# Kernel optimization log

Measured on AMD Instinct MI355X. Metric: run time of the kernel, lower is better.

Reference implementation:

```python
import jax, jax.numpy as jnp
import numpy as np

E = 8192   # line-graph nodes (edges of g)
N = 4096   # graph nodes
FIN = 64   # in_feats
FOUT = 64  # out_feats
H = FOUT // 2
BN_EPS = 1e-5


def _linear_params(k, fan_in):
    kw, kb = jax.random.split(k)
    s = 1.0 / np.sqrt(fan_in)
    w = jax.random.uniform(kw, (H, fan_in), jnp.float32, -s, s)
    b = jax.random.uniform(kb, (H,), jnp.float32, -s, s)
    return w, b


def setup_inputs() -> dict:
    key = jax.random.key(0)
    ks = jax.random.split(key, 12)
    inp = {}
    inp["y"] = jax.random.normal(ks[0], (E, FIN), jnp.float32)
    inp["deg_g"] = jax.random.uniform(ks[1], (N,), jnp.float32)  # unused in forward
    inp["g_a1"] = jnp.zeros((N, N), jnp.float32)                  # unused in forward
    # adjacency-like 0/1 matrices, sparse pattern stored dense (as th.mm expects)
    inp["lg_a1"] = (jax.random.uniform(ks[2], (E, E)) < (8.0 / E)).astype(jnp.float32)
    inp["pm"] = (jax.random.uniform(ks[3], (N, E)) < (2.0 / N)).astype(jnp.float32)
    inp["pd"] = (jax.random.uniform(ks[4], (N, E)) < (2.0 / N)).astype(jnp.float32)
    inp["theta_y_w"], inp["theta_y_b"] = _linear_params(ks[5], FIN)
    inp["theta_y_r_w"], inp["theta_y_r_b"] = _linear_params(ks[6], FIN)
    inp["gamma_a_w"], inp["gamma_a_b"] = _linear_params(ks[7], FIN)
    inp["gamma_x_w"], inp["gamma_x_b"] = _linear_params(ks[8], FOUT)
    inp["gamma_a_r_w"], inp["gamma_a_r_b"] = _linear_params(ks[9], FIN)
    inp["gamma_x_r_w"], inp["gamma_x_r_b"] = _linear_params(ks[10], FOUT)
    inp["bn_x_w"] = jnp.ones((FOUT,), jnp.float32)
    inp["bn_x_b"] = jnp.zeros((FOUT,), jnp.float32)
    inp["bn_y_w"] = jnp.ones((FOUT,), jnp.float32)
    inp["bn_y_b"] = jnp.zeros((FOUT,), jnp.float32)
    return inp


def _bn(x, w, b):
    # BatchNorm2d on [B, C, 1, 1] in training mode == per-channel batch norm
    # with biased variance over the row (batch) dimension.
    m = x.mean(0)
    v = jnp.mean((x - m) ** 2, axis=0)
    return (x - m) * jax.lax.rsqrt(v + BN_EPS) * w + b


def reference(y, deg_g, g_a1, lg_a1, pm, pd,
              theta_y_w, theta_y_b, theta_y_r_w, theta_y_r_b,
              gamma_a_w, gamma_a_b, gamma_x_w, gamma_x_b,
              gamma_a_r_w, gamma_a_r_b, gamma_x_r_w, gamma_x_r_b,
              bn_x_w, bn_x_b, bn_y_w, bn_y_b):
    pd_y = pd @ y                                        # [N, FIN]
    x_r = pd_y @ theta_y_r_w.T + theta_y_r_b             # [N, H]
    x = pd_y @ theta_y_w.T + theta_y_b                   # [N, H]
    x = jnp.concatenate([x, jax.nn.relu(x_r)], axis=1)   # [N, FOUT]
    x = _bn(x, bn_x_w, bn_x_b)
    pm_x = pm.T @ x                                      # [E, FOUT]
    lg_y = lg_a1 @ y                                     # [E, FIN] (computed once; torch computes it twice, same math)
    y_r = (lg_y @ gamma_a_r_w.T + gamma_a_r_b) + (pm_x @ gamma_x_r_w.T + gamma_x_r_b)
    y_n = (lg_y @ gamma_a_w.T + gamma_a_b) + (pm_x @ gamma_x_w.T + gamma_x_b)
    y_out = jnp.concatenate([y_n, jax.nn.relu(y_r)], axis=1)  # [E, FOUT]
    return _bn(y_out, bn_y_w, bn_y_b)
```

## Files before the change

### kernel.cpp

```cpp
#include <hip/hip_runtime.h>

typedef unsigned int uint_t;
typedef unsigned short ushort_t;
typedef unsigned long long ull_t;

#define SLOTS 48

__device__ __forceinline__ float bcast(float v, int k) {
    union { float f; int i; } x; x.f = v;
    int r = __builtin_amdgcn_readlane(x.i, k);
    union { int i; float f; } y2; y2.i = r;
    return y2.f;
}

__global__ __launch_bounds__(256) void stream_gather_kernel(
    const float* __restrict__ lg, const float* __restrict__ pd,
    const float* __restrict__ pm, const float* __restrict__ y,
    float* __restrict__ lg_y, float* __restrict__ pd_y,
    ushort_t* __restrict__ pm_keys, uint_t* __restrict__ pm_counts)
{
    __shared__ ushort_t sIdx[4][SLOTS];
    const int lane = threadIdx.x & 63;
    const int wv = threadIdx.x >> 6;
    const int wid = blockIdx.x * 4 + wv;
    const float* A;
    int row;
    if (wid < 8192)       { row = wid;         A = lg; }
    else if (wid < 12288) { row = wid - 8192;  A = pd; }
    else                  { row = wid - 12288; A = pm; }

    const uint4* ap = (const uint4*)(A + (size_t)row * 8192);
    ushort_t* slice = sIdx[wv];
    const ull_t lt = (1ull << lane) - 1ull;

    uint4 buf[8];
    #pragma unroll
    for (int i = 0; i < 8; ++i) buf[i] = ap[i * 64 + lane];

    uint_t cnt = 0;
    #pragma unroll
    for (int pp = 0; pp < 32; pp += 8) {
        #pragma unroll
        for (int i = 0; i < 8; ++i) {
            uint4 c = buf[i];
            if (pp + 8 + i < 32) buf[i] = ap[(pp + 8 + i) * 64 + lane];
            uint_t a0 = c.x, a1 = c.y, a2 = c.z, a3 = c.w;
            ull_t m = __ballot((a0 | a1 | a2 | a3) != 0u);
            if (m) {
                ull_t m0 = __ballot(a0 != 0u);
                ull_t m1 = __ballot(a1 != 0u);
                ull_t m2 = __ballot(a2 != 0u);
                ull_t m3 = __ballot(a3 != 0u);
                uint_t c0 = (uint_t)__popcll(m0), c1 = (uint_t)__popcll(m1);
                uint_t c2 = (uint_t)__popcll(m2);
                uint_t o0 = cnt + (uint_t)__popcll(m0 & lt);
                uint_t o1 = cnt + c0 + (uint_t)__popcll(m1 & lt);
                uint_t o2 = cnt + c0 + c1 + (uint_t)__popcll(m2 & lt);
                uint_t o3 = cnt + c0 + c1 + c2 + (uint_t)__popcll(m3 & lt);
                int j = (pp + i) * 256 + lane * 4;
                if (a0 && o0 < SLOTS) slice[o0] = (ushort_t)(j + 0);
                if (a1 && o1 < SLOTS) slice[o1] = (ushort_t)(j + 1);
                if (a2 && o2 < SLOTS) slice[o2] = (ushort_t)(j + 2);
                if (a3 && o3 < SLOTS) slice[o3] = (ushort_t)(j + 3);
                cnt += (uint_t)(__popcll(m0) + __popcll(m1) +
                                __popcll(m2) + __popcll(m3));
            }
        }
    }
    if (cnt > SLOTS) cnt = SLOTS;

    if (wid >= 12288) {
        if (lane == 0) pm_counts[row] = cnt;
        if (lane < (int)cnt) pm_keys[(size_t)row * SLOTS + lane] = slice[lane];
        return;
    }
    float a0 = 0.f, a1 = 0.f, a2 = 0.f, a3 = 0.f;
    uint_t i = 0;
    for (; i + 4 <= cnt; i += 4) {
        int j0 = slice[i + 0], j1 = slice[i + 1];
        int j2 = slice[i + 2], j3 = slice[i + 3];
        a0 += y[(size_t)j0 * 64 + lane];
        a1 += y[(size_t)j1 * 64 + lane];
        a2 += y[(size_t)j2 * 64 + lane];
        a3 += y[(size_t)j3 * 64 + lane];
    }
    for (; i < cnt; ++i) a0 += y[(size_t)slice[i] * 64 + lane];
    float acc = (a0 + a1) + (a2 + a3);
    if (wid < 8192) lg_y[(size_t)row * 64 + lane] = acc;
    else            pd_y[(size_t)row * 64 + lane] = acc;
}

__global__ __launch_bounds__(256) void xlin_kernel(
    const float* __restrict__ pd_y,
    const float* __restrict__ wt, const float* __restrict__ bt,
    const float* __restrict__ wr, const float* __restrict__ br,
    float* __restrict__ x_raw, float* __restrict__ stats_x)
{
    __shared__ float red[2][4][64];
    const int wave = threadIdx.x >> 6, lane = threadIdx.x & 63;
    const float* wsrc = (lane < 32) ? (wt + lane * 64) : (wr + (lane - 32) * 64);
    float wreg[64];
    const float4* wp = (const float4*)wsrc;
    #pragma unroll
    for (int q = 0; q < 16; ++q) {
        float4 t = wp[q];
        wreg[q * 4 + 0] = t.x; wreg[q * 4 + 1] = t.y;
        wreg[q * 4 + 2] = t.z; wreg[q * 4 + 3] = t.w;
    }
    float bias = (lane < 32) ? bt[lane] : br[lane - 32];
    float s1 = 0.f, s2 = 0.f;
    const int row0 = (blockIdx.x * 4 + wave) * 8;
    for (int r = 0; r < 8; ++r) {
        int row = row0 + r;
        float xv = pd_y[(size_t)row * 64 + lane];
        float acc = bias;
        #pragma unroll
        for (int k = 0; k < 64; ++k) acc = fmaf(bcast(xv, k), wreg[k], acc);
        if (lane >= 32) acc = fmaxf(acc, 0.f);
        x_raw[(size_t)row * 64 + lane] = acc;
        s1 += acc; s2 += acc * acc;
    }
    red[0][wave][lane] = s1; red[1][wave][lane] = s2;
    __syncthreads();
    if (wave == 0) {
        float a = 0.f, b = 0.f;
        #pragma unroll
        for (int w = 0; w < 4; ++w) { a += red[0][w][lane]; b += red[1][w][lane]; }
        atomicAdd(&stats_x[lane], a);
        atomicAdd(&stats_x[64 + lane], b);
    }
}

__global__ __launch_bounds__(256) void scatter_kernel(
    const ushort_t* __restrict__ pm_keys, const uint_t* __restrict__ pm_counts,
    const float* __restrict__ x_raw, const float* __restrict__ stats_x,
    const float* __restrict__ bnxw, const float* __restrict__ bnxb,
    float* __restrict__ pm_x)
{
    const int lane = threadIdx.x & 63;
    const int row = blockIdx.x * 4 + (threadIdx.x >> 6);
    float mean = stats_x[lane] * (1.f / 4096.f);
    float var  = fmaxf(stats_x[64 + lane] * (1.f / 4096.f) - mean * mean, 0.f);
    float rstd = rsqrtf(var + 1e-5f);
    float scale = rstd * bnxw[lane];
    float shift = bnxb[lane] - mean * scale;
    const ushort_t* slice = pm_keys + (size_t)row * SLOTS;
    uint_t cnt = pm_counts[row];
    float xb = fmaf(x_raw[(size_t)row * 64 + lane], scale, shift);
    for (uint_t i = 0; i < cnt; ++i) {
        int e = slice[i];
        atomicAdd(&pm_x[(size_t)e * 64 + lane], xb);
    }
}

__global__ __launch_bounds__(256) void ylin_kernel(
    const float* __restrict__ lg_y, const float* __restrict__ pm_x,
    const float* __restrict__ wa, const float* __restrict__ ba,
    const float* __restrict__ wx, const float* __restrict__ bx,
    const float* __restrict__ war, const float* __restrict__ bar,
    const float* __restrict__ wxr, const float* __restrict__ bxr,
    float* __restrict__ yraw, float* __restrict__ stats_y)
{
    __shared__ float red[2][4][64];
    const int wave = threadIdx.x >> 6, lane = threadIdx.x & 63;
    const float* s1p = (lane < 32) ? (wa + lane * 64) : (war + (lane - 32) * 64);
    const float* s2p = (lane < 32) ? (wx + lane * 64) : (wxr + (lane - 32) * 64);
    float w1[64], w2[64];
    {
        const float4* p1 = (const float4*)s1p;
        const float4* p2 = (const float4*)s2p;
        #pragma unroll
        for (int q = 0; q < 16; ++q) {
            float4 t1 = p1[q], t2 = p2[q];
            w1[q * 4 + 0] = t1.x; w1[q * 4 + 1] = t1.y;
            w1[q * 4 + 2] = t1.z; w1[q * 4 + 3] = t1.w;
            w2[q * 4 + 0] = t2.x; w2[q * 4 + 1] = t2.y;
            w2[q * 4 + 2] = t2.z; w2[q * 4 + 3] = t2.w;
        }
    }
    float bias = (lane < 32) ? (ba[lane] + bx[lane])
                             : (bar[lane - 32] + bxr[lane - 32]);
    float s1 = 0.f, s2 = 0.f;
    const int row0 = (blockIdx.x * 4 + wave) * 8;
    for (int r = 0; r < 8; ++r) {
        int row = row0 + r;
        float lv = lg_y[(size_t)row * 64 + lane];
        float pv = pm_x[(size_t)row * 64 + lane];
        float acc = bias;
        #pragma unroll
        for (int k = 0; k < 64; ++k) {
            acc = fmaf(bcast(lv, k), w1[k], acc);
            acc = fmaf(bcast(pv, k), w2[k], acc);
        }
        if (lane >= 32) acc = fmaxf(acc, 0.f);
        yraw[(size_t)row * 64 + lane] = acc;
        s1 += acc; s2 += acc * acc;
    }
    red[0][wave][lane] = s1; red[1][wave][lane] = s2;
    __syncthreads();
    if (wave == 0) {
        float a = 0.f, b = 0.f;
        #pragma unroll
        for (int w = 0; w < 4; ++w) { a += red[0][w][lane]; b += red[1][w][lane]; }
        atomicAdd(&stats_y[lane], a);
        atomicAdd(&stats_y[64 + lane], b);
    }
}

__global__ __launch_bounds__(256) void bny_kernel(
    float* __restrict__ yraw, const float* __restrict__ stats_y,
    const float* __restrict__ bnyw, const float* __restrict__ bnyb)
{
    int idx = blockIdx.x * 256 + threadIdx.x;
    int c = idx & 63;
    float mean = stats_y[c] * (1.f / 8192.f);
    float var  = fmaxf(stats_y[64 + c] * (1.f / 8192.f) - mean * mean, 0.f);
    float rstd = rsqrtf(var + 1e-5f);
    yraw[idx] = (yraw[idx] - mean) * rstd * bnyw[c] + bnyb[c];
}

extern "C" void kernel_launch(void* const* d_in, const int* in_sizes, int n_in,
                              void* d_out, int out_size, void* d_ws, size_t ws_size,
                              hipStream_t stream)
{
    const float* y     = (const float*)d_in[0];
    const float* lg_a1 = (const float*)d_in[3];
    const float* pm    = (const float*)d_in[4];
    const float* pd    = (const float*)d_in[5];
    const float* th_w  = (const float*)d_in[6];
    const float* th_b  = (const float*)d_in[7];
    const float* thr_w = (const float*)d_in[8];
    const float* thr_b = (const float*)d_in[9];
    const float* ga_w  = (const float*)d_in[10];
    const float* ga_b  = (const float*)d_in[11];
    const float* gx_w  = (const float*)d_in[12];
    const float* gx_b  = (const float*)d_in[13];
    const float* gar_w = (const float*)d_in[14];
    const float* gar_b = (const float*)d_in[15];
    const float* gxr_w = (const float*)d_in[16];
    const float* gxr_b = (const float*)d_in[17];
    const float* bnx_w = (const float*)d_in[18];
    const float* bnx_b = (const float*)d_in[19];
    const float* bny_w = (const float*)d_in[20];
    const float* bny_b = (const float*)d_in[21];

    char* ws = (char*)d_ws;
    float* stats_x = (float*)ws;
    float* stats_y = (float*)(ws + 1024);
    float* pm_x    = (float*)(ws + 2048);
    const size_t zero_bytes = 2048 + (size_t)8192 * 64 * 4;
    float* pd_y  = (float*)(ws + zero_bytes);
    float* lg_y  = pd_y + (size_t)4096 * 64;
    float* x_raw = lg_y + (size_t)8192 * 64;
    ushort_t* pm_keys = (ushort_t*)(x_raw + (size_t)4096 * 64);
    uint_t* pm_counts = (uint_t*)(pm_keys + (size_t)4096 * SLOTS);
    float* yraw  = (float*)d_out;

    hipMemsetAsync(d_ws, 0, zero_bytes, stream);

    stream_gather_kernel<<<4096, 256, 0, stream>>>(lg_a1, pd, pm, y,
                                                   lg_y, pd_y,
                                                   pm_keys, pm_counts);
    xlin_kernel<<<128, 256, 0, stream>>>(pd_y, th_w, th_b, thr_w, thr_b,
                                         x_raw, stats_x);
    scatter_kernel<<<1024, 256, 0, stream>>>(pm_keys, pm_counts, x_raw, stats_x,
                                             bnx_w, bnx_b, pm_x);
    ylin_kernel<<<256, 256, 0, stream>>>(lg_y, pm_x, ga_w, ga_b, gx_w, gx_b,
                                         gar_w, gar_b, gxr_w, gxr_b,
                                         yraw, stats_y);
    bny_kernel<<<2048, 256, 0, stream>>>(yraw, stats_y, bny_w, bny_b);
}
```

Before: 601.9 us.

## Interleave row scanning across waves and use nontemporal loads in stream gather

The dense-scan kernel now has the four waves of a block cooperatively stream four consecutive rows in interleaved 1 KB chunks instead of each wave owning one row. Per-row slot counters move to shared atomics, and a block barrier comes before the gather phase. Loads use nontemporal hints so the 512 MB of adjacency data does not pollute the cache, and SLOTS grows from 48 to 64. The goal is more sequential DRAM access across waves, at the cost of extra LDS atomics and synchronisation. Because slot order now depends on atomic order, the order of the float accumulation is no longer fixed.

New measurement: 576.0 us. -4.3%, faster.

```diff
diff --git a/kernel.cpp b/kernel.cpp
--- a/kernel.cpp
+++ b/kernel.cpp
@@ -3,8 +3,9 @@
 typedef unsigned int uint_t;
 typedef unsigned short ushort_t;
 typedef unsigned long long ull_t;
-
-#define SLOTS 48
+typedef uint_t nvec4 __attribute__((ext_vector_type(4)));
+
+#define SLOTS 64
 
 __device__ __forceinline__ float bcast(float v, int k) {
     union { float f; int i; } x; x.f = v;
@@ -19,31 +20,37 @@
     float* __restrict__ lg_y, float* __restrict__ pd_y,
     ushort_t* __restrict__ pm_keys, uint_t* __restrict__ pm_counts)
 {
-    __shared__ ushort_t sIdx[4][SLOTS];
+    __shared__ ushort_t sSlice[4][SLOTS];
+    __shared__ uint_t sCnt[4];
     const int lane = threadIdx.x & 63;
     const int wv = threadIdx.x >> 6;
-    const int wid = blockIdx.x * 4 + wv;
+    const int bid = blockIdx.x;
     const float* A;
-    int row;
-    if (wid < 8192)       { row = wid;         A = lg; }
-    else if (wid < 12288) { row = wid - 8192;  A = pd; }
-    else                  { row = wid - 12288; A = pm; }
-
-    const uint4* ap = (const uint4*)(A + (size_t)row * 8192);
-    ushort_t* slice = sIdx[wv];
+    int row0, mat;
+    if (bid < 2048)      { mat = 0; row0 = bid * 4;          A = lg; }
+    else if (bid < 3072) { mat = 1; row0 = (bid - 2048) * 4; A = pd; }
+    else                 { mat = 2; row0 = (bid - 3072) * 4; A = pm; }
+
+    if (threadIdx.x < 4) sCnt[threadIdx.x] = 0;
+    __syncthreads();
+
+    const nvec4* ap = (const nvec4*)(A + (size_t)row0 * 8192);
     const ull_t lt = (1ull << lane) - 1ull;
 
-    uint4 buf[8];
+    nvec4 buf[8];
     #pragma unroll
-    for (int i = 0; i < 8; ++i) buf[i] = ap[i * 64 + lane];
-
-    uint_t cnt = 0;
+    for (int i = 0; i < 8; ++i)
+        buf[i] = __builtin_nontemporal_load(ap + (size_t)(wv + 4 * i) * 64 + lane);
+
     #pragma unroll
     for (int pp = 0; pp < 32; pp += 8) {
         #pragma unroll
         for (int i = 0; i < 8; ++i) {
-            uint4 c = buf[i];
-            if (pp + 8 + i < 32) buf[i] = ap[(pp + 8 + i) * 64 + lane];
+            nvec4 c = buf[i];
+            if (pp + 8 + i < 32)
+                buf[i] = __builtin_nontemporal_load(
+                    ap + (size_t)(wv + 4 * (pp + 8 + i)) * 64 + lane);
+            const int g = wv + 4 * (pp + i);
             uint_t a0 = c.x, a1 = c.y, a2 = c.z, a3 = c.w;
             ull_t m = __ballot((a0 | a1 | a2 | a3) != 0u);
             if (m) {
@@ -52,42 +59,50 @@
                 ull_t m2 = __ballot(a2 != 0u);
                 ull_t m3 = __ballot(a3 != 0u);
                 uint_t c0 = (uint_t)__popcll(m0), c1 = (uint_t)__popcll(m1);
-                uint_t c2 = (uint_t)__popcll(m2);
-                uint_t o0 = cnt + (uint_t)__popcll(m0 & lt);
-                uint_t o1 = cnt + c0 + (uint_t)__popcll(m1 & lt);
-                uint_t o2 = cnt + c0 + c1 + (uint_t)__popcll(m2 & lt);
-                uint_t o3 = cnt + c0 + c1 + c2 + (uint_t)__popcll(m3 & lt);
-                int j = (pp + i) * 256 + lane * 4;
-                if (a0 && o0 < SLOTS) slice[o0] = (ushort_t)(j + 0);
-                if (a1 && o1 < SLOTS) slice[o1] = (ushort_t)(j + 1);
-                if (a2 && o2 < SLOTS) slice[o2] = (ushort_t)(j + 2);
-                if (a3 && o3 < SLOTS) slice[o3] = (ushort_t)(j + 3);
-                cnt += (uint_t)(__popcll(m0) + __popcll(m1) +
-                                __popcll(m2) + __popcll(m3));
+                uint_t c2 = (uint_t)__popcll(m2), c3 = (uint_t)__popcll(m3);
+                uint_t total = c0 + c1 + c2 + c3;
+                const int q = g >> 5;
+                uint_t base = 0;
+                if (lane == 0) base = atomicAdd(&sCnt[q], total);
+                base = (uint_t)__shfl((int)base, 0);
+                uint_t o0 = base + (uint_t)__popcll(m0 & lt);
+                uint_t o1 = base + c0 + (uint_t)__popcll(m1 & lt);
+                uint_t o2 = base + c0 + c1 + (uint_t)__popcll(m2 & lt);
+                uint_t o3 = base + c0 + c1 + c2 + (uint_t)__popcll(m3 & lt);
+                int jb = (g & 31) * 256 + lane * 4;
+                ushort_t* sl = sSlice[q];
+                if (a0 && o0 < SLOTS) sl[o0] = (ushort_t)(jb + 0);
+                if (a1 && o1 < SLOTS) sl[o1] = (ushort_t)(jb + 1);
+                if (a2 && o2 < SLOTS) sl[o2] = (ushort_t)(jb + 2);
+                if (a3 && o3 < SLOTS) sl[o3] = (ushort_t)(jb + 3);
             }
         }
     }
-    if (cnt > SLOTS) cnt = SLOTS;
-
-    if (wid >= 12288) {
+    __syncthreads();
+
+    const int row = row0 + wv;
+    uint_t cnt = sCnt[wv]; if (cnt > SLOTS) cnt = SLOTS;
+    const ushort_t* sl = sSlice[wv];
+
+    if (mat == 2) {
         if (lane == 0) pm_counts[row] = cnt;
-        if (lane < (int)cnt) pm_keys[(size_t)row * SLOTS + lane] = slice[lane];
+        if (lane < (int)cnt) pm_keys[(size_t)row * SLOTS + lane] = sl[lane];
         return;
     }
     float a0 = 0.f, a1 = 0.f, a2 = 0.f, a3 = 0.f;
     uint_t i = 0;
     for (; i + 4 <= cnt; i += 4) {
-        int j0 = slice[i + 0], j1 = slice[i + 1];
-        int j2 = slice[i + 2], j3 = slice[i + 3];
+        int j0 = sl[i + 0], j1 = sl[i + 1];
+        int j2 = sl[i + 2], j3 = sl[i + 3];
         a0 += y[(size_t)j0 * 64 + lane];
         a1 += y[(size_t)j1 * 64 + lane];
         a2 += y[(size_t)j2 * 64 + lane];
         a3 += y[(size_t)j3 * 64 + lane];
     }
-    for (; i < cnt; ++i) a0 += y[(size_t)slice[i] * 64 + lane];
+    for (; i < cnt; ++i) a0 += y[(size_t)sl[i] * 64 + lane];
     float acc = (a0 + a1) + (a2 + a3);
-    if (wid < 8192) lg_y[(size_t)row * 64 + lane] = acc;
-    else            pd_y[(size_t)row * 64 + lane] = acc;
+    if (mat == 0) lg_y[(size_t)row * 64 + lane] = acc;
+    else          pd_y[(size_t)row * 64 + lane] = acc;
 }
 
 __global__ __launch_bounds__(256) void xlin_kernel(
@@ -256,7 +271,7 @@
     uint_t* pm_counts = (uint_t*)(pm_keys + (size_t)4096 * SLOTS);
     float* yraw  = (float*)d_out;
 
-    hipMemsetAsync(d_ws, 0, zero_bytes, stream);
+    (void)hipMemsetAsync(d_ws, 0, zero_bytes, stream);
 
     stream_gather_kernel<<<4096, 256, 0, stream>>>(lg_a1, pd, pm, y,
                                                    lg_y, pd_y,
```
